# Kernel tuning notes

Hardware: AMD Instinct MI355X
Metric: run time of the kernel (lower is better)

Reference implementation:

```python
import jax, jax.numpy as jnp
import numpy as np

N_NODES = 100000
N_EDGES = 1600000
IN_CH = 128
HID_CH = 128


def setup_inputs() -> dict:
    key = jax.random.key(0)
    ks = jax.random.split(key, 10)
    x = jax.random.normal(ks[0], (N_NODES, IN_CH), dtype=jnp.float32)
    edge_index = jax.random.randint(ks[1], (2, N_EDGES), 0, N_NODES, dtype=jnp.int64)
    s1 = 1.0 / np.sqrt(IN_CH)
    s2 = 1.0 / np.sqrt(HID_CH)
    return {
        "x": x,
        "edge_index": edge_index,
        "W1": jax.random.uniform(ks[2], (IN_CH, HID_CH), jnp.float32, -s1, s1),
        "b1": jnp.zeros((HID_CH,), jnp.float32),
        "W2": jax.random.uniform(ks[3], (HID_CH, HID_CH), jnp.float32, -s2, s2),
        "b2": jnp.zeros((HID_CH,), jnp.float32),
        "We": jax.random.uniform(ks[4], (IN_CH, HID_CH), jnp.float32, -s1, s1),
        "be": jax.random.uniform(ks[5], (HID_CH,), jnp.float32, -s1, s1),
        "Wfc": jax.random.uniform(ks[6], (HID_CH, 1), jnp.float32, -s2, s2),
        "bfc": jax.random.uniform(ks[7], (1,), jnp.float32, -s2, s2),
    }


def _gcn_conv(x, src, dst, norm, W, b, n_nodes):
    # PyG GCNConv: linear transform, then normalized scatter-add aggregation, then bias
    h = x @ W                                 # [N, H]
    msg = h[src] * norm[:, None]              # gather + scale  [E+N, H]
    out = jax.ops.segment_sum(msg, dst, num_segments=n_nodes)  # scatter-add [N, H]
    return out + b


def reference(x, edge_index, W1, b1, W2, b2, We, be, Wfc, bfc):
    n = x.shape[0]
    # add self-loops (PyG default add_self_loops=True)
    loop = jnp.arange(n, dtype=edge_index.dtype)
    src = jnp.concatenate([edge_index[0], loop])
    dst = jnp.concatenate([edge_index[1], loop])
    # symmetric degree normalization deg^-1/2 (edge_weight implicitly ones)
    deg = jax.ops.segment_sum(jnp.ones_like(src, dtype=x.dtype), dst, num_segments=n)
    dinv = jnp.where(deg > 0, jax.lax.rsqrt(deg), 0.0)
    norm = dinv[src] * dinv[dst]

    x_conv = jax.nn.relu(_gcn_conv(x, src, dst, norm, W1, b1, n))
    x_fc = jax.nn.relu(x @ We + be)
    h = x_conv + x_fc                          # residual; dropout is identity in eval
    x_conv2 = jax.nn.relu(_gcn_conv(h, src, dst, norm, W2, b2, n))
    h = x_conv2 + h
    # batch is all zeros -> global_mean_pool == mean over all nodes -> [1, H]
    pooled = jnp.mean(h, axis=0, keepdims=True)
    predict = jax.nn.sigmoid(pooled @ Wfc + bfc)  # [1, 1]
    return predict
```

## Files before the change

kernel.cpp:

```cpp
#include <hip/hip_runtime.h>
#include <hip/hip_bf16.h>

typedef unsigned int uint;
typedef unsigned short ushort;
typedef unsigned char uchar;
typedef __attribute__((ext_vector_type(8))) short short8;
typedef __attribute__((ext_vector_type(4))) float f32x4;

__device__ __forceinline__ float bf2f(ushort u) {
    union { uint i; float f; } v; v.i = ((uint)u) << 16; return v.f;
}
__device__ __forceinline__ ushort f2bf(float f) {
    union { float f; uint i; } v; v.f = f;
    uint x = v.i;
    uint r = (x + 0x7FFFu + ((x >> 16) & 1u)) >> 16;
    return (ushort)r;
}
__device__ __forceinline__ uchar f2q(float f) {
    return (uchar)(__builtin_amdgcn_cvt_pk_fp8_f32(f, 0.f, 0, false) & 0xFF);
}
__device__ __forceinline__ void q2f4(uint w, float* o) {
    o[0] = __builtin_amdgcn_cvt_f32_fp8(w, 0);
    o[1] = __builtin_amdgcn_cvt_f32_fp8(w, 1);
    o[2] = __builtin_amdgcn_cvt_f32_fp8(w, 2);
    o[3] = __builtin_amdgcn_cvt_f32_fp8(w, 3);
}


__global__ void k_degree(const int* __restrict__ dst, int* __restrict__ deg,
                         int e, int n) {
    int bin = blockIdx.x & 7;
    int sub = blockIdx.x >> 3;
    int nsub = gridDim.x >> 3;
    int q = (n + 7) >> 3;
    int lo = bin * q, hi = min(n, lo + q);
    for (int i = sub * 256 + threadIdx.x; i < e; i += nsub * 256) {
        int d = dst[i];
        if (d >= lo && d < hi) atomicAdd(&deg[d], 1);
    }
}

__global__ void k_dinv(const int* __restrict__ deg, float* __restrict__ dinv, int n) {
    int i = blockIdx.x * 256 + threadIdx.x;
    if (i < n) dinv[i] = rsqrtf((float)deg[i] + 1.0f);
}

__global__ void k_scan_a(const int* __restrict__ deg, int* __restrict__ bsum, int n) {
    __shared__ int sd[256];
    int t = threadIdx.x;
    int base = blockIdx.x * 1024 + t * 4;
    int s = 0;
#pragma unroll
    for (int j = 0; j < 4; ++j) { int idx = base + j; if (idx < n) s += deg[idx]; }
    sd[t] = s; __syncthreads();
    for (int off = 1; off < 256; off <<= 1) {
        int v = (t >= off) ? sd[t - off] : 0;
        __syncthreads();
        sd[t] += v;
        __syncthreads();
    }
    if (t == 255) bsum[blockIdx.x] = sd[255];
}

__global__ void k_scan_b(const int* __restrict__ bsum, int* __restrict__ boff, int nb) {
    __shared__ int sd[256];
    int t = threadIdx.x;
    int v0 = (t < nb) ? bsum[t] : 0;
    sd[t] = v0; __syncthreads();
    for (int off = 1; off < 256; off <<= 1) {
        int v = (t >= off) ? sd[t - off] : 0;
        __syncthreads();
        sd[t] += v;
        __syncthreads();
    }
    if (t < nb) boff[t] = sd[t] - v0;
}

__global__ void k_scan_c(const int* __restrict__ deg, const int* __restrict__ boff,
                         int* __restrict__ offs, int n) {
    __shared__ int sd[256];
    int t = threadIdx.x;
    int base = blockIdx.x * 1024 + t * 4;
    int vals[4]; int s = 0;
#pragma unroll
    for (int j = 0; j < 4; ++j) {
        int idx = base + j;
        vals[j] = (idx < n) ? deg[idx] : 0;
        s += vals[j];
    }
    sd[t] = s; __syncthreads();
    for (int off = 1; off < 256; off <<= 1) {
        int v = (t >= off) ? sd[t - off] : 0;
        __syncthreads();
        sd[t] += v;
        __syncthreads();
    }
    int run = boff[blockIdx.x] + (sd[t] - s);
#pragma unroll
    for (int j = 0; j < 4; ++j) {
        int idx = base + j;
        if (idx < n) { offs[idx] = run; run += vals[j]; }
    }
}

__global__ void k_fill(const int* __restrict__ src, const int* __restrict__ dst,
                       const int* __restrict__ offs, int* __restrict__ cursor,
                       int* __restrict__ csr, int e, int n) {
    int bin = blockIdx.x & 7;
    int sub = blockIdx.x >> 3;
    int nsub = gridDim.x >> 3;
    int q = (n + 7) >> 3;
    int lo = bin * q, hi = min(n, lo + q);
    for (int i = sub * 256 + threadIdx.x; i < e; i += nsub * 256) {
        int d = dst[i];
        if (d >= lo && d < hi) {
            int p = offs[d] + atomicAdd(&cursor[d], 1);
            csr[p] = src[i];
        }
    }
}


__global__ __launch_bounds__(512) void k_gemm1(
    const float* __restrict__ x, const float* __restrict__ W1, const float* __restrict__ We,
    const float* __restrict__ be, const float* __restrict__ dinv,
    uchar* __restrict__ h1q, ushort* __restrict__ xfc, int n)
{
    __shared__ __align__(16) ushort Bt[256][72];
    int tid = threadIdx.x;
    int w = tid >> 6, lane = tid & 63;
    int ln15 = lane & 15, g = lane >> 4;
    int rowBase = blockIdx.x * 128 + w * 16;
    int r = rowBase + ln15;
    bool valid = r < n;

    short8 a[4];
#pragma unroll
    for (int ks = 0; ks < 4; ++ks) {
        float4 f0 = make_float4(0.f, 0.f, 0.f, 0.f), f1 = f0;
        if (valid) {
            const float* p = x + (size_t)r * 128 + ks * 32 + g * 8;
            f0 = *reinterpret_cast<const float4*>(p);
            f1 = *reinterpret_cast<const float4*>(p + 4);
        }
        short8 v;
        v[0] = (short)f2bf(f0.x); v[1] = (short)f2bf(f0.y);
        v[2] = (short)f2bf(f0.z); v[3] = (short)f2bf(f0.w);
        v[4] = (short)f2bf(f1.x); v[5] = (short)f2bf(f1.y);
        v[6] = (short)f2bf(f1.z); v[7] = (short)f2bf(f1.w);
        a[ks] = v;
    }

    f32x4 acc[16];
#pragma unroll
    for (int i = 0; i < 16; ++i) acc[i] = (f32x4){0.f, 0.f, 0.f, 0.f};

    for (int s = 0; s < 2; ++s) {
        for (int i = tid; i < 8192; i += 512) {
            int kl = i >> 7, j = i & 127;
            int kg = s * 64 + kl;
            Bt[j][kl]       = f2bf(W1[kg * 128 + j]);
            Bt[128 + j][kl] = f2bf(We[kg * 128 + j]);
        }
        __syncthreads();
#pragma unroll
        for (int t2 = 0; t2 < 2; ++t2) {
            short8 af = a[s * 2 + t2];
#pragma unroll
            for (int jf = 0; jf < 16; ++jf) {
                short8 bf = *reinterpret_cast<const short8*>(&Bt[jf * 16 + ln15][t2 * 32 + g * 8]);
                acc[jf] = __builtin_amdgcn_mfma_f32_16x16x32_bf16(af, bf, acc[jf], 0, 0, 0);
            }
        }
        __syncthreads();
    }

    float dv[4];
#pragma unroll
    for (int q = 0; q < 4; ++q) {
        int rr = rowBase + g * 4 + q;
        dv[q] = (rr < n) ? dinv[rr] : 0.f;
    }

#pragma unroll
    for (int jf = 0; jf < 16; ++jf) {
        int col = jf * 16 + ln15;
#pragma unroll
        for (int q = 0; q < 4; ++q) {
            int rr = rowBase + g * 4 + q;
            if (rr < n) {
                float v = acc[jf][q];
                if (col < 128) {
                    h1q[(size_t)rr * 128 + col] = f2q(v * dv[q]);
                } else {
                    float vv = fmaxf(v + be[col - 128], 0.f);
                    xfc[(size_t)rr * 128 + (col - 128)] = f2bf(vv);
                }
            }
        }
    }
}


__global__ __launch_bounds__(512) void k_gemm2(
    const ushort* __restrict__ h, const float* __restrict__ W2, const float* __restrict__ dinv,
    uchar* __restrict__ h2q, int n)
{
    __shared__ __align__(16) ushort Bt[128][72];
    int tid = threadIdx.x;
    int w = tid >> 6, lane = tid & 63;
    int ln15 = lane & 15, g = lane >> 4;
    int rowBase = blockIdx.x * 128 + w * 16;
    int r = rowBase + ln15;
    bool valid = r < n;

    short8 a[4];
#pragma unroll
    for (int ks = 0; ks < 4; ++ks) {
        short8 v = (short8){0,0,0,0,0,0,0,0};
        if (valid) v = *reinterpret_cast<const short8*>(h + (size_t)r * 128 + ks * 32 + g * 8);
        a[ks] = v;
    }

    f32x4 acc[8];
#pragma unroll
    for (int i = 0; i < 8; ++i) acc[i] = (f32x4){0.f, 0.f, 0.f, 0.f};

    for (int s = 0; s < 2; ++s) {
        for (int i = tid; i < 8192; i += 512) {
            int kl = i >> 7, j = i & 127;
            Bt[j][kl] = f2bf(W2[(s * 64 + kl) * 128 + j]);
        }
        __syncthreads();
#pragma unroll
        for (int t2 = 0; t2 < 2; ++t2) {
            short8 af = a[s * 2 + t2];
#pragma unroll
            for (int jf = 0; jf < 8; ++jf) {
                short8 bf = *reinterpret_cast<const short8*>(&Bt[jf * 16 + ln15][t2 * 32 + g * 8]);
                acc[jf] = __builtin_amdgcn_mfma_f32_16x16x32_bf16(af, bf, acc[jf], 0, 0, 0);
            }
        }
        __syncthreads();
    }

    float dv[4];
#pragma unroll
    for (int q = 0; q < 4; ++q) {
        int rr = rowBase + g * 4 + q;
        dv[q] = (rr < n) ? dinv[rr] : 0.f;
    }

#pragma unroll
    for (int jf = 0; jf < 8; ++jf) {
        int col = jf * 16 + ln15;
#pragma unroll
        for (int q = 0; q < 4; ++q) {
            int rr = rowBase + g * 4 + q;
            if (rr < n) h2q[(size_t)rr * 128 + col] = f2q(acc[jf][q] * dv[q]);
        }
    }
}


__global__ __launch_bounds__(256) void k_agg1(
    const int* __restrict__ csr, const int* __restrict__ offs, const int* __restrict__ degE,
    const float* __restrict__ dinv, const uchar* __restrict__ h1q, const ushort* __restrict__ xfc,
    const float* __restrict__ b1, ushort* __restrict__ h, int n)
{
    int t = threadIdx.x;
    int g = t >> 4, li = t & 15;
    int node = blockIdx.x * 16 + g;
    if (node >= n) return;
    int off = offs[node], cnt = degE[node];
    float di = dinv[node];
    int c0 = li * 8;
    const uchar* tbl = h1q + c0;
    float acc[8];
#pragma unroll
    for (int e = 0; e < 8; ++e) acc[e] = 0.f;

    for (int base = 0; base < cnt; base += 8) {
        uint2 u[8];
#pragma unroll
        for (int q = 0; q < 8; ++q) {
            int s = csr[off + base + q];
            int id = (base + q < cnt) ? s : n;
            u[q] = *reinterpret_cast<const uint2*>(tbl + (size_t)id * 128);
        }
#pragma unroll
        for (int q = 0; q < 8; ++q) {
            float d4[4];
            q2f4(u[q].x, d4);
            acc[0] += d4[0]; acc[1] += d4[1]; acc[2] += d4[2]; acc[3] += d4[3];
            q2f4(u[q].y, d4);
            acc[4] += d4[0]; acc[5] += d4[1]; acc[6] += d4[2]; acc[7] += d4[3];
        }
    }

    uint2 us = *reinterpret_cast<const uint2*>(tbl + (size_t)node * 128);
    float sdec[8];
    q2f4(us.x, sdec); q2f4(us.y, sdec + 4);
    uint4 ux = *reinterpret_cast<const uint4*>(xfc + (size_t)node * 128 + c0);
    uint uxw[4] = {ux.x, ux.y, ux.z, ux.w};
    float4 bA = *reinterpret_cast<const float4*>(b1 + c0);
    float4 bB = *reinterpret_cast<const float4*>(b1 + c0 + 4);
    float bb[8] = {bA.x, bA.y, bA.z, bA.w, bB.x, bB.y, bB.z, bB.w};
    uint outw[4];
#pragma unroll
    for (int j = 0; j < 4; ++j) {
        int e0 = 2 * j, e1 = 2 * j + 1;
        float v0 = fmaxf((acc[e0] + sdec[e0]) * di + bb[e0], 0.f) + bf2f((ushort)(uxw[j] & 0xffff));
        float v1 = fmaxf((acc[e1] + sdec[e1]) * di + bb[e1], 0.f) + bf2f((ushort)(uxw[j] >> 16));
        outw[j] = (uint)f2bf(v0) | ((uint)f2bf(v1) << 16);
    }
    *reinterpret_cast<uint4*>(h + (size_t)node * 128 + c0) =
        make_uint4(outw[0], outw[1], outw[2], outw[3]);
}


__global__ __launch_bounds__(256) void k_agg2(
    const int* __restrict__ csr, const int* __restrict__ offs, const int* __restrict__ degE,
    const float* __restrict__ dinv, const uchar* __restrict__ h2q, const ushort* __restrict__ hres,
    const float* __restrict__ b2, float* __restrict__ pooled, int n)
{
    __shared__ float lpool[128];
    int t = threadIdx.x;
    if (t < 128) lpool[t] = 0.f;
    __syncthreads();
    int g = t >> 4, li = t & 15;
    int node = blockIdx.x * 16 + g;
    bool valid = node < n;
    int nodeC = valid ? node : (n - 1);
    int off = offs[nodeC];
    int cnt = valid ? degE[nodeC] : 0;
    float di = dinv[nodeC];
    int c0 = li * 8;
    const uchar* tbl = h2q + c0;
    float acc[8];
#pragma unroll
    for (int e = 0; e < 8; ++e) acc[e] = 0.f;

    for (int base = 0; base < cnt; base += 8) {
        uint2 u[8];
#pragma unroll
        for (int q = 0; q < 8; ++q) {
            int s = csr[off + base + q];
            int id = (base + q < cnt) ? s : n;
            u[q] = *reinterpret_cast<const uint2*>(tbl + (size_t)id * 128);
        }
#pragma unroll
        for (int q = 0; q < 8; ++q) {
            float d4[4];
            q2f4(u[q].x, d4);
            acc[0] += d4[0]; acc[1] += d4[1]; acc[2] += d4[2]; acc[3] += d4[3];
            q2f4(u[q].y, d4);
            acc[4] += d4[0]; acc[5] += d4[1]; acc[6] += d4[2]; acc[7] += d4[3];
        }
    }

    uint2 us = *reinterpret_cast<const uint2*>(tbl + (size_t)nodeC * 128);
    float sdec[8];
    q2f4(us.x, sdec); q2f4(us.y, sdec + 4);
    uint4 ur = *reinterpret_cast<const uint4*>(hres + (size_t)nodeC * 128 + c0);
    uint urw[4] = {ur.x, ur.y, ur.z, ur.w};
    float4 bA = *reinterpret_cast<const float4*>(b2 + c0);
    float4 bB = *reinterpret_cast<const float4*>(b2 + c0 + 4);
    float bb[8] = {bA.x, bA.y, bA.z, bA.w, bB.x, bB.y, bB.z, bB.w};
    float pv[8];
#pragma unroll
    for (int j = 0; j < 4; ++j) {
        int e0 = 2 * j, e1 = 2 * j + 1;
        float v0 = fmaxf((acc[e0] + sdec[e0]) * di + bb[e0], 0.f) + bf2f((ushort)(urw[j] & 0xffff));
        float v1 = fmaxf((acc[e1] + sdec[e1]) * di + bb[e1], 0.f) + bf2f((ushort)(urw[j] >> 16));
        pv[e0] = valid ? v0 : 0.f;
        pv[e1] = valid ? v1 : 0.f;
    }
#pragma unroll
    for (int e = 0; e < 8; ++e) {
        pv[e] += __shfl_xor(pv[e], 16);
        pv[e] += __shfl_xor(pv[e], 32);
    }
    if ((t & 63) < 16) {
#pragma unroll
        for (int e = 0; e < 8; ++e) atomicAdd(&lpool[c0 + e], pv[e]);
    }
    __syncthreads();
    if (t < 128) atomicAdd(&pooled[t], lpool[t]);
}


__global__ void k_final(const float* __restrict__ pooled, const float* __restrict__ Wfc,
                        const float* __restrict__ bfc, float* __restrict__ out, float invN) {
    int lane = threadIdx.x;
    float s = pooled[2 * lane] * invN * Wfc[2 * lane] +
              pooled[2 * lane + 1] * invN * Wfc[2 * lane + 1];
#pragma unroll
    for (int off = 32; off > 0; off >>= 1) s += __shfl_down(s, off);
    if (lane == 0) out[0] = 1.f / (1.f + expf(-(s + bfc[0])));
}


extern "C" void kernel_launch(void* const* d_in, const int* in_sizes, int n_in,
                              void* d_out, int out_size, void* d_ws, size_t ws_size,
                              hipStream_t stream) {
    const float* x   = (const float*)d_in[0];
    const int*   ei  = (const int*)d_in[1];
    const float* W1  = (const float*)d_in[2];
    const float* b1  = (const float*)d_in[3];
    const float* W2  = (const float*)d_in[4];
    const float* b2  = (const float*)d_in[5];
    const float* We  = (const float*)d_in[6];
    const float* be  = (const float*)d_in[7];
    const float* Wfc = (const float*)d_in[8];
    const float* bfc = (const float*)d_in[9];
    float* out = (float*)d_out;

    const int N = in_sizes[0] / 128;
    const int E = in_sizes[1] / 2;
    const int* src = ei;
    const int* dst = ei + E;

    char* w = (char*)d_ws;
    size_t off = 0;
    auto take = [&](size_t bytes) -> void* {
        void* p = w + off;
        off = (off + bytes + 255) & ~(size_t)255;
        return p;
    };
    int*    deg    = (int*)take((size_t)N * 4);
    int*    offs   = (int*)take((size_t)N * 4);
    int*    cursor = (int*)take((size_t)N * 4);
    float*  dinv   = (float*)take((size_t)N * 4);
    int*    bsum   = (int*)take(1024);
    int*    boff   = (int*)take(1024);
    int*    csr    = (int*)take((size_t)(E + 64) * 4);
    uchar*  h1q    = (uchar*)take((size_t)(N + 1) * 128);
    ushort* xfc    = (ushort*)take((size_t)N * 128 * 2);
    ushort* h      = (ushort*)take((size_t)N * 128 * 2);
    uchar*  h2q    = (uchar*)take((size_t)(N + 1) * 128);
    float*  pooled = (float*)take(512);

    const int nbScan = (N + 1023) / 1024;

    hipMemsetAsync(deg, 0, (size_t)N * 4, stream);
    hipMemsetAsync(cursor, 0, (size_t)N * 4, stream);
    hipMemsetAsync(pooled, 0, 512, stream);
    hipMemsetAsync(h1q + (size_t)N * 128, 0, 128, stream);
    hipMemsetAsync(h2q + (size_t)N * 128, 0, 128, stream);

    k_degree<<<2048, 256, 0, stream>>>(dst, deg, E, N);
    k_dinv<<<(N + 255) / 256, 256, 0, stream>>>(deg, dinv, N);
    k_scan_a<<<nbScan, 256, 0, stream>>>(deg, bsum, N);
    k_scan_b<<<1, 256, 0, stream>>>(bsum, boff, nbScan);
    k_scan_c<<<nbScan, 256, 0, stream>>>(deg, boff, offs, N);
    k_fill<<<2048, 256, 0, stream>>>(src, dst, offs, cursor, csr, E, N);

    k_gemm1<<<(N + 127) / 128, 512, 0, stream>>>(x, W1, We, be, dinv, h1q, xfc, N);
    k_agg1<<<(N + 15) / 16, 256, 0, stream>>>(csr, offs, deg, dinv, h1q, xfc, b1, h, N);
    k_gemm2<<<(N + 127) / 128, 512, 0, stream>>>(h, W2, dinv, h2q, N);
    k_agg2<<<(N + 15) / 16, 256, 0, stream>>>(csr, offs, deg, dinv, h2q, h, b2, pooled, N);
    k_final<<<1, 64, 0, stream>>>(pooled, Wfc, bfc, out, 1.0f / (float)N);
}
```

Baseline: 440.9 us.

## Split fp8 feature tables into column slices for cache-friendly aggregation

The fp8 h1q/h2q tables are stored as four 32-column slices, each of size (N+1)x32, instead of row-major 128-wide rows. The aggregation kernels now launch four chunked passes, one per slice, with two threads per node each gathering 16 bytes. The aim is a smaller working set per pass (about 3.2MB per slice) so gathered rows stay resident in cache. In exchange the CSR index stream is read four times, and the pooling now issues LDS atomics per element. Nontemporal loads and stores are added for streaming data.

```diff
diff --git a/kernel.cpp b/kernel.cpp
--- a/kernel.cpp
+++ b/kernel.cpp
@@ -6,6 +6,7 @@
 typedef unsigned char uchar;
 typedef __attribute__((ext_vector_type(8))) short short8;
 typedef __attribute__((ext_vector_type(4))) float f32x4;
+typedef __attribute__((ext_vector_type(4))) uint u32x4;
 
 __device__ __forceinline__ float bf2f(ushort u) {
     union { uint i; float f; } v; v.i = ((uint)u) << 16; return v.f;
@@ -133,6 +134,7 @@
     int rowBase = blockIdx.x * 128 + w * 16;
     int r = rowBase + ln15;
     bool valid = r < n;
+    size_t slice = (size_t)(n + 1) * 32;
 
     short8 a[4];
 #pragma unroll
@@ -191,7 +193,7 @@
             if (rr < n) {
                 float v = acc[jf][q];
                 if (col < 128) {
-                    h1q[(size_t)rr * 128 + col] = f2q(v * dv[q]);
+                    h1q[(size_t)(col >> 5) * slice + (size_t)rr * 32 + (col & 31)] = f2q(v * dv[q]);
                 } else {
                     float vv = fmaxf(v + be[col - 128], 0.f);
                     xfc[(size_t)rr * 128 + (col - 128)] = f2bf(vv);
@@ -213,6 +215,7 @@
     int rowBase = blockIdx.x * 128 + w * 16;
     int r = rowBase + ln15;
     bool valid = r < n;
+    size_t slice = (size_t)(n + 1) * 32;
 
     short8 a[4];
 #pragma unroll
@@ -257,7 +260,8 @@
 #pragma unroll
         for (int q = 0; q < 4; ++q) {
             int rr = rowBase + g * 4 + q;
-            if (rr < n) h2q[(size_t)rr * 128 + col] = f2q(acc[jf][q] * dv[q]);
+            if (rr < n)
+                h2q[(size_t)(col >> 5) * slice + (size_t)rr * 32 + (col & 31)] = f2q(acc[jf][q] * dv[q]);
         }
     }
 }
@@ -266,127 +270,138 @@
 __global__ __launch_bounds__(256) void k_agg1(
     const int* __restrict__ csr, const int* __restrict__ offs, const int* __restrict__ degE,
     const float* __restrict__ dinv, const uchar* __restrict__ h1q, const ushort* __restrict__ xfc,
-    const float* __restrict__ b1, ushort* __restrict__ h, int n)
+    const float* __restrict__ b1, ushort* __restrict__ h, int n, int nodeBlocks)
 {
     int t = threadIdx.x;
-    int g = t >> 4, li = t & 15;
-    int node = blockIdx.x * 16 + g;
+    int chunk = blockIdx.x / nodeBlocks;
+    int nb = blockIdx.x - chunk * nodeBlocks;
+    int pair = t >> 1, sub = t & 1;
+    int node = nb * 128 + pair;
     if (node >= n) return;
+    size_t slice = (size_t)(n + 1) * 32;
+    const uchar* tbl = h1q + (size_t)chunk * slice + sub * 16;
     int off = offs[node], cnt = degE[node];
     float di = dinv[node];
-    int c0 = li * 8;
-    const uchar* tbl = h1q + c0;
-    float acc[8];
-#pragma unroll
-    for (int e = 0; e < 8; ++e) acc[e] = 0.f;
+    float acc[16];
+#pragma unroll
+    for (int e = 0; e < 16; ++e) acc[e] = 0.f;
 
     for (int base = 0; base < cnt; base += 8) {
-        uint2 u[8];
+        u32x4 u[8];
 #pragma unroll
         for (int q = 0; q < 8; ++q) {
-            int s = csr[off + base + q];
+            int s = __builtin_nontemporal_load(csr + off + base + q);
             int id = (base + q < cnt) ? s : n;
-            u[q] = *reinterpret_cast<const uint2*>(tbl + (size_t)id * 128);
+            u[q] = *reinterpret_cast<const u32x4*>(tbl + (size_t)id * 32);
         }
 #pragma unroll
         for (int q = 0; q < 8; ++q) {
             float d4[4];
-            q2f4(u[q].x, d4);
-            acc[0] += d4[0]; acc[1] += d4[1]; acc[2] += d4[2]; acc[3] += d4[3];
-            q2f4(u[q].y, d4);
-            acc[4] += d4[0]; acc[5] += d4[1]; acc[6] += d4[2]; acc[7] += d4[3];
-        }
-    }
-
-    uint2 us = *reinterpret_cast<const uint2*>(tbl + (size_t)node * 128);
-    float sdec[8];
-    q2f4(us.x, sdec); q2f4(us.y, sdec + 4);
-    uint4 ux = *reinterpret_cast<const uint4*>(xfc + (size_t)node * 128 + c0);
-    uint uxw[4] = {ux.x, ux.y, ux.z, ux.w};
-    float4 bA = *reinterpret_cast<const float4*>(b1 + c0);
-    float4 bB = *reinterpret_cast<const float4*>(b1 + c0 + 4);
-    float bb[8] = {bA.x, bA.y, bA.z, bA.w, bB.x, bB.y, bB.z, bB.w};
-    uint outw[4];
-#pragma unroll
-    for (int j = 0; j < 4; ++j) {
+            q2f4(u[q][0], d4); acc[0] += d4[0]; acc[1] += d4[1]; acc[2] += d4[2]; acc[3] += d4[3];
+            q2f4(u[q][1], d4); acc[4] += d4[0]; acc[5] += d4[1]; acc[6] += d4[2]; acc[7] += d4[3];
+            q2f4(u[q][2], d4); acc[8] += d4[0]; acc[9] += d4[1]; acc[10] += d4[2]; acc[11] += d4[3];
+            q2f4(u[q][3], d4); acc[12] += d4[0]; acc[13] += d4[1]; acc[14] += d4[2]; acc[15] += d4[3];
+        }
+    }
+
+    u32x4 us = *reinterpret_cast<const u32x4*>(tbl + (size_t)node * 32);
+    float sdec[16];
+    q2f4(us[0], sdec); q2f4(us[1], sdec + 4); q2f4(us[2], sdec + 8); q2f4(us[3], sdec + 12);
+    int c0 = chunk * 32 + sub * 16;
+    const u32x4* xp = reinterpret_cast<const u32x4*>(xfc + (size_t)node * 128 + c0);
+    u32x4 x0 = __builtin_nontemporal_load(xp);
+    u32x4 x1 = __builtin_nontemporal_load(xp + 1);
+    uint xw[8] = {x0[0], x0[1], x0[2], x0[3], x1[0], x1[1], x1[2], x1[3]};
+    float bb[16];
+#pragma unroll
+    for (int p = 0; p < 4; ++p) {
+        float4 bq = *reinterpret_cast<const float4*>(b1 + c0 + p * 4);
+        bb[4 * p] = bq.x; bb[4 * p + 1] = bq.y; bb[4 * p + 2] = bq.z; bb[4 * p + 3] = bq.w;
+    }
+    uint outw[8];
+#pragma unroll
+    for (int j = 0; j < 8; ++j) {
         int e0 = 2 * j, e1 = 2 * j + 1;
-        float v0 = fmaxf((acc[e0] + sdec[e0]) * di + bb[e0], 0.f) + bf2f((ushort)(uxw[j] & 0xffff));
-        float v1 = fmaxf((acc[e1] + sdec[e1]) * di + bb[e1], 0.f) + bf2f((ushort)(uxw[j] >> 16));
+        float v0 = fmaxf((acc[e0] + sdec[e0]) * di + bb[e0], 0.f) + bf2f((ushort)(xw[j] & 0xffff));
+        float v1 = fmaxf((acc[e1] + sdec[e1]) * di + bb[e1], 0.f) + bf2f((ushort)(xw[j] >> 16));
         outw[j] = (uint)f2bf(v0) | ((uint)f2bf(v1) << 16);
     }
-    *reinterpret_cast<uint4*>(h + (size_t)node * 128 + c0) =
-        make_uint4(outw[0], outw[1], outw[2], outw[3]);
+    ushort* hp = h + (size_t)node * 128 + c0;
+    u32x4 o0 = {outw[0], outw[1], outw[2], outw[3]};
+    u32x4 o1 = {outw[4], outw[5], outw[6], outw[7]};
+    __builtin_nontemporal_store(o0, reinterpret_cast<u32x4*>(hp));
+    __builtin_nontemporal_store(o1, reinterpret_cast<u32x4*>(hp + 8));
 }
 
 
 __global__ __launch_bounds__(256) void k_agg2(
     const int* __restrict__ csr, const int* __restrict__ offs, const int* __restrict__ degE,
     const float* __restrict__ dinv, const uchar* __restrict__ h2q, const ushort* __restrict__ hres,
-    const float* __restrict__ b2, float* __restrict__ pooled, int n)
+    const float* __restrict__ b2, float* __restrict__ pooled, int n, int nodeBlocks)
 {
     __shared__ float lpool[128];
     int t = threadIdx.x;
     if (t < 128) lpool[t] = 0.f;
     __syncthreads();
-    int g = t >> 4, li = t & 15;
-    int node = blockIdx.x * 16 + g;
+    int chunk = blockIdx.x / nodeBlocks;
+    int nb = blockIdx.x - chunk * nodeBlocks;
+    int pair = t >> 1, sub = t & 1;
+    int node = nb * 128 + pair;
     bool valid = node < n;
     int nodeC = valid ? node : (n - 1);
+    size_t slice = (size_t)(n + 1) * 32;
+    const uchar* tbl = h2q + (size_t)chunk * slice + sub * 16;
     int off = offs[nodeC];
     int cnt = valid ? degE[nodeC] : 0;
     float di = dinv[nodeC];
-    int c0 = li * 8;
-    const uchar* tbl = h2q + c0;
-    float acc[8];
-#pragma unroll
-    for (int e = 0; e < 8; ++e) acc[e] = 0.f;
+    float acc[16];
+#pragma unroll
+    for (int e = 0; e < 16; ++e) acc[e] = 0.f;
 
     for (int base = 0; base < cnt; base += 8) {
-        uint2 u[8];
+        u32x4 u[8];
 #pragma unroll
         for (int q = 0; q < 8; ++q) {
-            int s = csr[off + base + q];
+            int s = __builtin_nontemporal_load(csr + off + base + q);
             int id = (base + q < cnt) ? s : n;
-            u[q] = *reinterpret_cast<const uint2*>(tbl + (size_t)id * 128);
+            u[q] = *reinterpret_cast<const u32x4*>(tbl + (size_t)id * 32);
         }
 #pragma unroll
         for (int q = 0; q < 8; ++q) {
             float d4[4];
-            q2f4(u[q].x, d4);
-            acc[0] += d4[0]; acc[1] += d4[1]; acc[2] += d4[2]; acc[3] += d4[3];
-            q2f4(u[q].y, d4);
-            acc[4] += d4[0]; acc[5] += d4[1]; acc[6] += d4[2]; acc[7] += d4[3];
-        }
-    }
-
-    uint2 us = *reinterpret_cast<const uint2*>(tbl + (size_t)nodeC * 128);
-    float sdec[8];
-    q2f4(us.x, sdec); q2f4(us.y, sdec + 4);
-    uint4 ur = *reinterpret_cast<const uint4*>(hres + (size_t)nodeC * 128 + c0);
-    uint urw[4] = {ur.x, ur.y, ur.z, ur.w};
-    float4 bA = *reinterpret_cast<const float4*>(b2 + c0);
-    float4 bB = *reinterpret_cast<const float4*>(b2 + c0 + 4);
-    float bb[8] = {bA.x, bA.y, bA.z, bA.w, bB.x, bB.y, bB.z, bB.w};
-    float pv[8];
-#pragma unroll
-    for (int j = 0; j < 4; ++j) {
-        int e0 = 2 * j, e1 = 2 * j + 1;
-        float v0 = fmaxf((acc[e0] + sdec[e0]) * di + bb[e0], 0.f) + bf2f((ushort)(urw[j] & 0xffff));
-        float v1 = fmaxf((acc[e1] + sdec[e1]) * di + bb[e1], 0.f) + bf2f((ushort)(urw[j] >> 16));
-        pv[e0] = valid ? v0 : 0.f;
-        pv[e1] = valid ? v1 : 0.f;
-    }
-#pragma unroll
-    for (int e = 0; e < 8; ++e) {
-        pv[e] += __shfl_xor(pv[e], 16);
-        pv[e] += __shfl_xor(pv[e], 32);
-    }
-    if ((t & 63) < 16) {
-#pragma unroll
-        for (int e = 0; e < 8; ++e) atomicAdd(&lpool[c0 + e], pv[e]);
+            q2f4(u[q][0], d4); acc[0] += d4[0]; acc[1] += d4[1]; acc[2] += d4[2]; acc[3] += d4[3];
+            q2f4(u[q][1], d4); acc[4] += d4[0]; acc[5] += d4[1]; acc[6] += d4[2]; acc[7] += d4[3];
+            q2f4(u[q][2], d4); acc[8] += d4[0]; acc[9] += d4[1]; acc[10] += d4[2]; acc[11] += d4[3];
+            q2f4(u[q][3], d4); acc[12] += d4[0]; acc[13] += d4[1]; acc[14] += d4[2]; acc[15] += d4[3];
+        }
+    }
+
+    u32x4 us = *reinterpret_cast<const u32x4*>(tbl + (size_t)nodeC * 32);
+    float sdec[16];
+    q2f4(us[0], sdec); q2f4(us[1], sdec + 4); q2f4(us[2], sdec + 8); q2f4(us[3], sdec + 12);
+    int c0 = chunk * 32 + sub * 16;
+    const u32x4* rp = reinterpret_cast<const u32x4*>(hres + (size_t)nodeC * 128 + c0);
+    u32x4 r0 = __builtin_nontemporal_load(rp);
+    u32x4 r1 = __builtin_nontemporal_load(rp + 1);
+    uint rw[8] = {r0[0], r0[1], r0[2], r0[3], r1[0], r1[1], r1[2], r1[3]};
+    float bb[16];
+#pragma unroll
+    for (int p = 0; p < 4; ++p) {
+        float4 bq = *reinterpret_cast<const float4*>(b2 + c0 + p * 4);
+        bb[4 * p] = bq.x; bb[4 * p + 1] = bq.y; bb[4 * p + 2] = bq.z; bb[4 * p + 3] = bq.w;
+    }
+    if (valid) {
+#pragma unroll
+        for (int j = 0; j < 8; ++j) {
+            int e0 = 2 * j, e1 = 2 * j + 1;
+            float v0 = fmaxf((acc[e0] + sdec[e0]) * di + bb[e0], 0.f) + bf2f((ushort)(rw[j] & 0xffff));
+            float v1 = fmaxf((acc[e1] + sdec[e1]) * di + bb[e1], 0.f) + bf2f((ushort)(rw[j] >> 16));
+            atomicAdd(&lpool[c0 + e0], v0);
+            atomicAdd(&lpool[c0 + e1], v1);
+        }
     }
     __syncthreads();
-    if (t < 128) atomicAdd(&pooled[t], lpool[t]);
+    if (t < 32) atomicAdd(&pooled[chunk * 32 + t], lpool[chunk * 32 + t]);
 }
 
 
@@ -441,13 +456,17 @@
     uchar*  h2q    = (uchar*)take((size_t)(N + 1) * 128);
     float*  pooled = (float*)take(512);
 
+    const size_t slice = (size_t)(N + 1) * 32;
     const int nbScan = (N + 1023) / 1024;
+    const int nodeBlocks = (N + 127) / 128;
 
     hipMemsetAsync(deg, 0, (size_t)N * 4, stream);
     hipMemsetAsync(cursor, 0, (size_t)N * 4, stream);
     hipMemsetAsync(pooled, 0, 512, stream);
-    hipMemsetAsync(h1q + (size_t)N * 128, 0, 128, stream);
-    hipMemsetAsync(h2q + (size_t)N * 128, 0, 128, stream);
+    for (int p = 0; p < 4; ++p) {
+        hipMemsetAsync(h1q + p * slice + (size_t)N * 32, 0, 32, stream);
+        hipMemsetAsync(h2q + p * slice + (size_t)N * 32, 0, 32, stream);
+    }
 
     k_degree<<<2048, 256, 0, stream>>>(dst, deg, E, N);
     k_dinv<<<(N + 255) / 256, 256, 0, stream>>>(deg, dinv, N);
@@ -457,8 +476,8 @@
     k_fill<<<2048, 256, 0, stream>>>(src, dst, offs, cursor, csr, E, N);
 
     k_gemm1<<<(N + 127) / 128, 512, 0, stream>>>(x, W1, We, be, dinv, h1q, xfc, N);
-    k_agg1<<<(N + 15) / 16, 256, 0, stream>>>(csr, offs, deg, dinv, h1q, xfc, b1, h, N);
+    k_agg1<<<4 * nodeBlocks, 256, 0, stream>>>(csr, offs, deg, dinv, h1q, xfc, b1, h, N, nodeBlocks);
     k_gemm2<<<(N + 127) / 128, 512, 0, stream>>>(h, W2, dinv, h2q, N);
-    k_agg2<<<(N + 15) / 16, 256, 0, stream>>>(csr, offs, deg, dinv, h2q, h, b2, pooled, N);
+    k_agg2<<<4 * nodeBlocks, 256, 0, stream>>>(csr, offs, deg, dinv, h2q, h, b2, pooled, N, nodeBlocks);
     k_final<<<1, 64, 0, stream>>>(pooled, Wfc, bfc, out, 1.0f / (float)N);
 }
```

New measurement: 448.0 us. No clear change (+1.6%).
